# Optimization experiments

Measured on AMD Instinct MI355X. Metric: run time of the kernel, lower is better.

The kernel has to match this reference:

```python
import jax, jax.numpy as jnp
import numpy as np

B, S = 16, 512
IN_DIM, ATTN_DIM, DEPTH, HEADS, DH = 512, 512, 4, 8, 64
CB_DIM, CB_SIZE, MAX_SEQ = 64, 8192, 544


def _ln(x, g, b):
    mu = x.mean(-1, keepdims=True)
    v = ((x - mu) ** 2).mean(-1, keepdims=True)
    return (x - mu) / jnp.sqrt(v + 1e-5) * g + b


def setup_inputs() -> dict:
    key = jax.random.key(0)
    ks = jax.random.split(key, 16)
    sc = 0.02
    d = {
        "x": jax.random.normal(ks[0], (B, S, IN_DIM), jnp.float32),
        "w_in": jax.random.normal(ks[1], (IN_DIM, ATTN_DIM), jnp.float32) * sc,
        "b_in": jnp.zeros((ATTN_DIM,), jnp.float32),
        "pos_emb": jax.random.normal(ks[2], (MAX_SEQ, ATTN_DIM), jnp.float32) * sc,
        "ln1_g": jnp.ones((DEPTH, ATTN_DIM), jnp.float32),
        "ln1_b": jnp.zeros((DEPTH, ATTN_DIM), jnp.float32),
        "wq": jax.random.normal(ks[3], (DEPTH, ATTN_DIM, ATTN_DIM), jnp.float32) * sc,
        "wk": jax.random.normal(ks[4], (DEPTH, ATTN_DIM, ATTN_DIM), jnp.float32) * sc,
        "wv": jax.random.normal(ks[5], (DEPTH, ATTN_DIM, ATTN_DIM), jnp.float32) * sc,
        "wo": jax.random.normal(ks[6], (DEPTH, ATTN_DIM, ATTN_DIM), jnp.float32) * sc,
        "ln2_g": jnp.ones((DEPTH, ATTN_DIM), jnp.float32),
        "ln2_b": jnp.zeros((DEPTH, ATTN_DIM), jnp.float32),
        "ff_w1": jax.random.normal(ks[7], (DEPTH, ATTN_DIM, 4 * ATTN_DIM), jnp.float32) * sc,
        "ff_b1": jnp.zeros((DEPTH, 4 * ATTN_DIM), jnp.float32),
        "ff_w2": jax.random.normal(ks[8], (DEPTH, 4 * ATTN_DIM, ATTN_DIM), jnp.float32) * sc,
        "ff_b2": jnp.zeros((DEPTH, ATTN_DIM), jnp.float32),
        "lnf_g": jnp.ones((ATTN_DIM,), jnp.float32),
        "lnf_b": jnp.zeros((ATTN_DIM,), jnp.float32),
        "w_out": jax.random.normal(ks[9], (ATTN_DIM, CB_DIM), jnp.float32) * sc,
        "b_out": jnp.zeros((CB_DIM,), jnp.float32),
        "codebook": jax.random.normal(ks[10], (CB_SIZE, CB_DIM), jnp.float32),
    }
    return d


def _attn(h, wq, wk, wv, wo):
    b, s, _ = h.shape
    q = jnp.einsum('bsd,de->bse', h, wq).reshape(b, s, HEADS, DH)
    k = jnp.einsum('bsd,de->bse', h, wk).reshape(b, s, HEADS, DH)
    v = jnp.einsum('bsd,de->bse', h, wv).reshape(b, s, HEADS, DH)
    scores = jnp.einsum('bqhd,bkhd->bhqk', q, k) * (DH ** -0.5)
    a = jax.nn.softmax(scores, axis=-1)
    o = jnp.einsum('bhqk,bkhd->bqhd', a, v).reshape(b, s, ATTN_DIM)
    return jnp.einsum('bse,ed->bsd', o, wo)


def reference(x, w_in, b_in, pos_emb, ln1_g, ln1_b, wq, wk, wv, wo,
              ln2_g, ln2_b, ff_w1, ff_b1, ff_w2, ff_b2, lnf_g, lnf_b,
              w_out, b_out, codebook):
    s = x.shape[1]
    # ContinuousTransformerWrapper: project in + absolute pos emb
    h = jnp.einsum('bsd,de->bse', x, w_in) + b_in + pos_emb[:s]
    # pre-norm encoder layers: attn + ff, each residual
    for i in range(DEPTH):
        h = h + _attn(_ln(h, ln1_g[i], ln1_b[i]), wq[i], wk[i], wv[i], wo[i])
        g = _ln(h, ln2_g[i], ln2_b[i])
        g = jax.nn.gelu(jnp.einsum('bsd,df->bsf', g, ff_w1[i]) + ff_b1[i])
        h = h + jnp.einsum('bsf,fd->bsd', g, ff_w2[i]) + ff_b2[i]
    h = _ln(h, lnf_g, lnf_b)
    z = jnp.einsum('bsd,dc->bsc', h, w_out) + b_out  # [B,S,CB_DIM]
    # VectorQuantize: euclidean nearest codebook entry
    d2 = (z ** 2).sum(-1, keepdims=True) - 2.0 * jnp.einsum('bsc,kc->bsk', z, codebook) \
         + (codebook ** 2).sum(-1)  # [B,S,CB_SIZE]
    idx = jnp.argmin(d2, axis=-1)
    q = codebook[idx]  # [B,S,CB_DIM]
    commit_loss = jnp.mean((jax.lax.stop_gradient(q) - z) ** 2)  # commitment_weight=1.0
    q_st = z + jax.lax.stop_gradient(q - z)  # straight-through
    return q_st.sum(axis=1), commit_loss
```

## Files before the change

### kernel.cpp

```cpp
#include <hip/hip_runtime.h>
#include <cmath>

#define BATCH 16
#define SEQ 512
#define DMODEL 512
#define NDEPTH 4
#define NHEADS 8
#define DHEAD 64
#define DFF 2048
#define CBD 64
#define CBS 8192
#define MROWS (BATCH * SEQ)

typedef unsigned short u16;
typedef __attribute__((ext_vector_type(8))) short short8;
typedef __attribute__((ext_vector_type(4))) float f32x4;
typedef __attribute__((ext_vector_type(4))) unsigned short u16x4;

__device__ __forceinline__ u16 f2bf(float f) {
    unsigned u = __float_as_uint(f);
    u += 0x7fff + ((u >> 16) & 1);
    return (u16)(u >> 16);
}
__device__ __forceinline__ float bf2f(u16 h) {
    return __uint_as_float(((unsigned)h) << 16);
}

__device__ __forceinline__ void async16(u16* lds, const u16* g) {
    __builtin_amdgcn_global_load_lds(
        (const __attribute__((address_space(1))) unsigned int*)g,
        (__attribute__((address_space(3))) unsigned int*)lds, 16, 0, 0);
}

__device__ __forceinline__ float gelu_tanh(float u) {
    float t = fmaf(0.07135481627f * u, u * u, 1.5957691216f * u);
    return u / (1.0f + __expf(-t));
}

__global__ void zero_kernel(float* __restrict__ p, int n) {
    int i = blockIdx.x * 256 + threadIdx.x;
    if (i < n) p[i] = 0.0f;
}

__global__ void cbn_kernel(const float* __restrict__ cb, float* __restrict__ cbn) {
    int c = blockIdx.x * 256 + threadIdx.x;
    if (c >= CBS) return;
    const float* row = cb + (size_t)c * CBD;
    float s = 0.0f;
#pragma unroll
    for (int d = 0; d < CBD; ++d) s += row[d] * row[d];
    cbn[c] = s;
}

__global__ __launch_bounds__(256) void wtrans_kernel(
    const float* __restrict__ W, u16* __restrict__ Th, u16* __restrict__ Tl,
    int K, int N, long inLS, long outLS) {
    __shared__ float t[32][33];
    const float* Ws = W + (size_t)blockIdx.z * inLS;
    u16* Tho = Th + (size_t)blockIdx.z * outLS;
    u16* Tlo = Tl + (size_t)blockIdx.z * outLS;
    int n0 = blockIdx.x * 32, k0 = blockIdx.y * 32;
    int tx = threadIdx.x & 31, ty = threadIdx.x >> 5;
#pragma unroll
    for (int r = ty; r < 32; r += 8) t[r][tx] = Ws[(size_t)(k0 + r) * N + n0 + tx];
    __syncthreads();
#pragma unroll
    for (int r = ty; r < 32; r += 8) {
        float v = t[tx][r];
        size_t o = (size_t)(n0 + r) * K + k0 + tx;
        u16 hh = f2bf(v);
        Tho[o] = hh;
        Tlo[o] = f2bf(v - bf2f(hh));
    }
}

__global__ __launch_bounds__(256) void vtrans_kernel(
    const u16* __restrict__ Qh, const u16* __restrict__ Ql,
    u16* __restrict__ VTh, u16* __restrict__ VTl) {
    __shared__ u16 t[64][68];
    int s0 = blockIdx.x * 64;
    int hh = blockIdx.y;
    int b = blockIdx.z & 15, plane = blockIdx.z >> 4;
    const u16* src = (plane ? Ql : Qh) + ((size_t)(16 + hh) * MROWS) * 64;
    u16* dst = (plane ? VTl : VTh);
    int tid = threadIdx.x;
    int rr = tid >> 4, c4 = (tid & 15) * 4;
#pragma unroll
    for (int i = 0; i < 4; ++i) {
        int r = rr + i * 16;
        const u16* p = src + (size_t)(b * SEQ + s0 + r) * 64 + c4;
        *(u16x4*)(&t[r][c4]) = *(const u16x4*)p;
    }
    __syncthreads();
#pragma unroll
    for (int i = 0; i < 4; ++i) {
        int r = rr + i * 16;
        u16x4 v;
        v.x = t[c4 + 0][r]; v.y = t[c4 + 1][r]; v.z = t[c4 + 2][r]; v.w = t[c4 + 3][r];
        *(u16x4*)(dst + (size_t)b * SEQ * DMODEL + (size_t)(hh * 64 + r) * SEQ + s0 + c4) = v;
    }
}

__global__ void split_kernel(const float* __restrict__ X, u16* __restrict__ H,
                             u16* __restrict__ L, int n) {
    int i = blockIdx.x * 256 + threadIdx.x;
    if (i < n) {
        float v = X[i];
        u16 hh = f2bf(v);
        H[i] = hh;
        L[i] = f2bf(v - bf2f(hh));
    }
}

__global__ __launch_bounds__(256) void ln_kernel(
    const float* __restrict__ X,
    const float* __restrict__ C0, const float* __restrict__ C1,
    const float* __restrict__ bias2, const float* __restrict__ pos2,
    float* __restrict__ Xout,
    float* __restrict__ Y, u16* __restrict__ Yh, u16* __restrict__ Yl,
    const float* __restrict__ g, const float* __restrict__ b) {
    int row  = blockIdx.x * 4 + (threadIdx.x >> 6);
    int lane = threadIdx.x & 63;
    float v[8];
    float s = 0.0f;
#pragma unroll
    for (int j = 0; j < 8; ++j) {
        int d = lane + j * 64;
        size_t o = (size_t)row * DMODEL + d;
        float t = X ? X[o] : 0.0f;
        if (C0)    t += C0[o] + C1[o];
        if (bias2) t += bias2[d];
        if (pos2)  t += pos2[(size_t)(row & (SEQ - 1)) * DMODEL + d];
        v[j] = t;
        if (Xout) Xout[o] = t;
        s += t;
    }
#pragma unroll
    for (int off = 32; off; off >>= 1) s += __shfl_xor(s, off);
    float mu  = s * (1.0f / DMODEL);
    float var = 0.0f;
#pragma unroll
    for (int j = 0; j < 8; ++j) { float d = v[j] - mu; var += d * d; }
#pragma unroll
    for (int off = 32; off; off >>= 1) var += __shfl_xor(var, off);
    float r = rsqrtf(var * (1.0f / DMODEL) + 1e-5f);
#pragma unroll
    for (int j = 0; j < 8; ++j) {
        int d = lane + j * 64;
        float y = (v[j] - mu) * r * g[d] + b[d];
        size_t o = (size_t)row * DMODEL + d;
        if (Y) Y[o] = y;
        if (Yh) {
            u16 hh = f2bf(y);
            Yh[o] = hh;
            Yl[o] = f2bf(y - bf2f(hh));
        }
    }
}

__global__ __launch_bounds__(256) void gemm3_kernel(
    const u16* __restrict__ Ah, const u16* __restrict__ Al,
    const u16* __restrict__ Bh, const u16* __restrict__ Bl,
    float* __restrict__ Cf, u16* __restrict__ Ch, u16* __restrict__ Cl,
    const float* __restrict__ bias, const float* __restrict__ res,
    const float* __restrict__ pos, int M, int N, int K, int gelu,
    float* __restrict__ Cs0, float* __restrict__ Cs1, int kslice, int qkvscatter) {
    __shared__ __align__(16) u16 AsH[128 * 64];
    __shared__ __align__(16) u16 AsL[128 * 64];
    __shared__ __align__(16) u16 BsH[128 * 64];
    __shared__ __align__(16) u16 BsL[128 * 64];

    int tid  = threadIdx.x;
    int w    = tid >> 6, lane = tid & 63;
    int wr   = w >> 1, wc = w & 1;
    int quad = lane >> 4, l16 = lane & 15;
    int m0   = blockIdx.x * 128;
    int n0   = blockIdx.y * 128;
    int ksA  = (kslice > 0) ? blockIdx.z * kslice : 0;
    int ksB  = (kslice > 0) ? ksA + kslice : K;

    f32x4 acc[4][4];
#pragma unroll
    for (int i = 0; i < 4; ++i)
#pragma unroll
        for (int j = 0; j < 4; ++j) acc[i][j] = (f32x4){0.f, 0.f, 0.f, 0.f};

    int ldsoff[4];
    size_t goff[4];
#pragma unroll
    for (int r = 0; r < 4; ++r) {
        int cidx = tid + 256 * r;
        int row = cidx >> 3;
        int cg = (cidx & 7) ^ (row & 7);
        ldsoff[r] = cidx * 8;
        goff[r] = (size_t)row * K + cg * 8;
    }

    const u16* AbaseH = Ah + (size_t)m0 * K;
    const u16* AbaseL = Al + (size_t)m0 * K;
    const u16* BbaseH = Bh + (size_t)n0 * K;
    const u16* BbaseL = Bl + (size_t)n0 * K;

    for (int ks = ksA; ks < ksB; ks += 64) {
        __syncthreads();
#pragma unroll
        for (int r = 0; r < 4; ++r) {
            size_t g = goff[r] + ks;
            async16(&AsH[ldsoff[r]], AbaseH + g);
            async16(&AsL[ldsoff[r]], AbaseL + g);
            async16(&BsH[ldsoff[r]], BbaseH + g);
            async16(&BsL[ldsoff[r]], BbaseL + g);
        }
        __syncthreads();
#pragma unroll
        for (int s = 0; s < 2; ++s) {
            short8 afh[4], afl[4];
#pragma unroll
            for (int i = 0; i < 4; ++i) {
                int row = wr * 64 + i * 16 + l16;
                int off = row * 64 + (((s << 2) | quad) ^ (row & 7)) * 8;
                afh[i] = *(const short8*)&AsH[off];
                afl[i] = *(const short8*)&AsL[off];
            }
#pragma unroll
            for (int j = 0; j < 4; ++j) {
                int rowb = wc * 64 + j * 16 + l16;
                int offb = rowb * 64 + (((s << 2) | quad) ^ (rowb & 7)) * 8;
                short8 bh = *(const short8*)&BsH[offb];
                short8 bl = *(const short8*)&BsL[offb];
#pragma unroll
                for (int i = 0; i < 4; ++i) {
                    acc[i][j] = __builtin_amdgcn_mfma_f32_16x16x32_bf16(afh[i], bh, acc[i][j], 0, 0, 0);
                    acc[i][j] = __builtin_amdgcn_mfma_f32_16x16x32_bf16(afl[i], bh, acc[i][j], 0, 0, 0);
                    acc[i][j] = __builtin_amdgcn_mfma_f32_16x16x32_bf16(afh[i], bl, acc[i][j], 0, 0, 0);
                }
            }
        }
    }

    float* Cspl = (kslice > 0) ? (blockIdx.z ? Cs1 : Cs0) : nullptr;
    int mbase = m0 + wr * 64;
    int nbase = n0 + wc * 64;
#pragma unroll
    for (int mi = 0; mi < 4; ++mi)
#pragma unroll
        for (int ni = 0; ni < 4; ++ni) {
            f32x4 a = acc[mi][ni];
#pragma unroll
            for (int r = 0; r < 4; ++r) {
                int m = mbase + mi * 16 + quad * 4 + r;
                int n = nbase + ni * 16 + l16;
                float v = a[r];
                size_t o = qkvscatter
                    ? ((size_t)(n >> 6) * M + m) * 64 + (n & 63)
                    : (size_t)m * N + n;
                if (Cspl) { Cspl[o] = v; continue; }
                if (bias) v += bias[n];
                if (pos)  v += pos[(size_t)(m & (SEQ - 1)) * N + n];
                if (res)  v += res[(size_t)m * N + n];
                if (gelu) v = gelu_tanh(v);
                if (Cf) Cf[o] = v;
                if (Ch) {
                    u16 hh = f2bf(v);
                    Ch[o] = hh;
                    Cl[o] = f2bf(v - bf2f(hh));
                }
            }
        }
}

__global__ __launch_bounds__(256) void gemm_kernel(
    const float* __restrict__ A, const float* __restrict__ Bm,
    float* __restrict__ C, const float* __restrict__ bias,
    int M, int N, int K) {
    __shared__ float As[16][68];
    __shared__ float Bs[16][64];
    int tid = threadIdx.x;
    int tx = tid & 15, ty = tid >> 4;
    int a_m = tid >> 2, a_k = (tid & 3) * 4;
    int b_k = tid >> 4, b_n = (tid & 15) * 4;
    const float* Arow = A + (size_t)(blockIdx.x * 64 + a_m) * K;
    const float* Bcol = Bm + (size_t)blockIdx.y * 64 + b_n;
    float acc[4][4] = {};
    for (int k0 = 0; k0 < K; k0 += 16) {
        float4 av = *(const float4*)(Arow + k0 + a_k);
        float4 bv = *(const float4*)(Bcol + (size_t)(k0 + b_k) * N);
        __syncthreads();
        As[a_k + 0][a_m] = av.x; As[a_k + 1][a_m] = av.y;
        As[a_k + 2][a_m] = av.z; As[a_k + 3][a_m] = av.w;
        *(float4*)(&Bs[b_k][b_n]) = bv;
        __syncthreads();
#pragma unroll
        for (int kk = 0; kk < 16; ++kk) {
            float4 a4 = *(const float4*)(&As[kk][ty * 4]);
            float4 b4 = *(const float4*)(&Bs[kk][tx * 4]);
            float ar[4] = {a4.x, a4.y, a4.z, a4.w};
            float br[4] = {b4.x, b4.y, b4.z, b4.w};
#pragma unroll
            for (int i = 0; i < 4; ++i)
#pragma unroll
                for (int j = 0; j < 4; ++j) acc[i][j] = fmaf(ar[i], br[j], acc[i][j]);
        }
    }
    int m0 = blockIdx.x * 64 + ty * 4;
    int n0 = blockIdx.y * 64 + tx * 4;
#pragma unroll
    for (int i = 0; i < 4; ++i) {
        float vv[4];
#pragma unroll
        for (int j = 0; j < 4; ++j) {
            float t = acc[i][j];
            if (bias) t += bias[n0 + j];
            vv[j] = t;
        }
        *(float4*)(C + (size_t)(m0 + i) * N + n0) = make_float4(vv[0], vv[1], vv[2], vv[3]);
    }
}

__global__ __launch_bounds__(256) void attn_flash_kernel(
    const u16* __restrict__ QKh, const u16* __restrict__ QKl,
    const u16* __restrict__ VTh, const u16* __restrict__ VTl,
    u16* __restrict__ Oh, u16* __restrict__ Ol) {
    int bh = blockIdx.x & 127;
    int qt = blockIdx.x >> 7;
    int bb = bh >> 3, hh = bh & 7;

    __shared__ __align__(16) float Pw[4][16 * 68];

    int tid = threadIdx.x;
    int w = tid >> 6, lane = tid & 63;
    int quad = lane >> 4, l16 = lane & 15;
    int qtile = qt * 4 + w;
    float* P = Pw[w];

    const u16* qrh = QKh + ((size_t)hh * MROWS + bb * SEQ + qtile * 16 + l16) * 64 + quad * 8;
    const u16* qrl = QKl + ((size_t)hh * MROWS + bb * SEQ + qtile * 16 + l16) * 64 + quad * 8;
    short8 Qh0 = *(const short8*)qrh;
    short8 Qh1 = *(const short8*)(qrh + 32);
    short8 Ql0 = *(const short8*)qrl;
    short8 Ql1 = *(const short8*)(qrl + 32);

    float m[4] = {-1e30f, -1e30f, -1e30f, -1e30f};
    float lsum[4] = {0.f, 0.f, 0.f, 0.f};
    f32x4 acc[4];
#pragma unroll
    for (int dt = 0; dt < 4; ++dt) acc[dt] = (f32x4){0.f, 0.f, 0.f, 0.f};

    const u16* KbH = QKh + ((size_t)(8 + hh) * MROWS + bb * SEQ) * 64;
    const u16* KbL = QKl + ((size_t)(8 + hh) * MROWS + bb * SEQ) * 64;
    const u16* VbH = VTh + (size_t)bb * SEQ * DMODEL + (size_t)(hh * 64) * SEQ;
    const u16* VbL = VTl + (size_t)bb * SEQ * DMODEL + (size_t)(hh * 64) * SEQ;

    for (int kt = 0; kt < 8; ++kt) {
        int kb = kt * 64;
        f32x4 st[4];
#pragma unroll
        for (int s = 0; s < 4; ++s) {
            const u16* kh = KbH + (size_t)(kb + s * 16 + l16) * 64 + quad * 8;
            const u16* kl = KbL + (size_t)(kb + s * 16 + l16) * 64 + quad * 8;
            short8 Kh0 = *(const short8*)kh;
            short8 Kh1 = *(const short8*)(kh + 32);
            short8 Kl0 = *(const short8*)kl;
            short8 Kl1 = *(const short8*)(kl + 32);
            f32x4 a = (f32x4){0.f, 0.f, 0.f, 0.f};
            a = __builtin_amdgcn_mfma_f32_16x16x32_bf16(Qh0, Kh0, a, 0, 0, 0);
            a = __builtin_amdgcn_mfma_f32_16x16x32_bf16(Qh1, Kh1, a, 0, 0, 0);
            a = __builtin_amdgcn_mfma_f32_16x16x32_bf16(Ql0, Kh0, a, 0, 0, 0);
            a = __builtin_amdgcn_mfma_f32_16x16x32_bf16(Ql1, Kh1, a, 0, 0, 0);
            a = __builtin_amdgcn_mfma_f32_16x16x32_bf16(Qh0, Kl0, a, 0, 0, 0);
            a = __builtin_amdgcn_mfma_f32_16x16x32_bf16(Qh1, Kl1, a, 0, 0, 0);
            st[s] = a * 0.125f;
        }
        float alpha[4];
#pragma unroll
        for (int r = 0; r < 4; ++r) {
            float mx = fmaxf(fmaxf(st[0][r], st[1][r]), fmaxf(st[2][r], st[3][r]));
#pragma unroll
            for (int off = 8; off; off >>= 1) mx = fmaxf(mx, __shfl_xor(mx, off));
            float mn = fmaxf(m[r], mx);
            alpha[r] = __expf(m[r] - mn);
            m[r] = mn;
        }
#pragma unroll
        for (int r = 0; r < 4; ++r) {
            float rs = 0.f;
#pragma unroll
            for (int s = 0; s < 4; ++s) {
                float p = __expf(st[s][r] - m[r]);
                st[s][r] = p;
                rs += p;
            }
#pragma unroll
            for (int off = 8; off; off >>= 1) rs += __shfl_xor(rs, off);
            lsum[r] = lsum[r] * alpha[r] + rs;
        }
#pragma unroll
        for (int dt = 0; dt < 4; ++dt)
#pragma unroll
            for (int r = 0; r < 4; ++r) acc[dt][r] *= alpha[r];
#pragma unroll
        for (int s = 0; s < 4; ++s)
#pragma unroll
            for (int r = 0; r < 4; ++r)
                P[(quad * 4 + r) * 68 + s * 16 + l16] = st[s][r];
        short8 ph[2], pl[2];
#pragma unroll
        for (int ks = 0; ks < 2; ++ks) {
            const float* src = &P[l16 * 68 + ks * 32 + quad * 8];
            f32x4 a0 = *(const f32x4*)src;
            f32x4 a1 = *(const f32x4*)(src + 4);
            float v[8] = {a0[0], a0[1], a0[2], a0[3], a1[0], a1[1], a1[2], a1[3]};
#pragma unroll
            for (int j = 0; j < 8; ++j) {
                u16 hv = f2bf(v[j]);
                ph[ks][j] = (short)hv;
                pl[ks][j] = (short)f2bf(v[j] - bf2f(hv));
            }
        }
#pragma unroll
        for (int dt = 0; dt < 4; ++dt) {
            const u16* vh = VbH + (size_t)(dt * 16 + l16) * SEQ + kb + quad * 8;
            const u16* vl = VbL + (size_t)(dt * 16 + l16) * SEQ + kb + quad * 8;
            short8 Vh0 = *(const short8*)vh;
            short8 Vh1 = *(const short8*)(vh + 32);
            short8 Vl0 = *(const short8*)vl;
            short8 Vl1 = *(const short8*)(vl + 32);
            acc[dt] = __builtin_amdgcn_mfma_f32_16x16x32_bf16(ph[0], Vh0, acc[dt], 0, 0, 0);
            acc[dt] = __builtin_amdgcn_mfma_f32_16x16x32_bf16(ph[1], Vh1, acc[dt], 0, 0, 0);
            acc[dt] = __builtin_amdgcn_mfma_f32_16x16x32_bf16(pl[0], Vh0, acc[dt], 0, 0, 0);
            acc[dt] = __builtin_amdgcn_mfma_f32_16x16x32_bf16(pl[1], Vh1, acc[dt], 0, 0, 0);
            acc[dt] = __builtin_amdgcn_mfma_f32_16x16x32_bf16(ph[0], Vl0, acc[dt], 0, 0, 0);
            acc[dt] = __builtin_amdgcn_mfma_f32_16x16x32_bf16(ph[1], Vl1, acc[dt], 0, 0, 0);
        }
    }

#pragma unroll
    for (int r = 0; r < 4; ++r) {
        float inv = 1.0f / lsum[r];
        size_t rowoff = (size_t)(bb * SEQ + qtile * 16 + quad * 4 + r) * DMODEL + hh * 64;
#pragma unroll
        for (int dt = 0; dt < 4; ++dt) {
            float v = acc[dt][r] * inv;
            u16 hv = f2bf(v);
            Oh[rowoff + dt * 16 + l16] = hv;
            Ol[rowoff + dt * 16 + l16] = f2bf(v - bf2f(hv));
        }
    }
}

__global__ __launch_bounds__(256) void vq3_kernel(
    const float* __restrict__ Z, const u16* __restrict__ Zh, const u16* __restrict__ Zl,
    const u16* __restrict__ CBh, const u16* __restrict__ CBl,
    const float* __restrict__ CB, const float* __restrict__ CBN,
    float* __restrict__ out) {
    __shared__ float sbest[4][16];
    __shared__ int sidx[4][16];
    __shared__ int ibest[16];
    __shared__ float psum[4][64];
    __shared__ float cl4[4];

    int tid = threadIdx.x;
    int w = tid >> 6, lane = tid & 63;
    int quad = lane >> 4, l16 = lane & 15;
    int row0 = blockIdx.x * 16;

    const u16* zph = Zh + (size_t)(row0 + l16) * CBD + quad * 8;
    const u16* zpl = Zl + (size_t)(row0 + l16) * CBD + quad * 8;
    short8 Z0h = *(const short8*)zph;
    short8 Z1h = *(const short8*)(zph + 32);
    short8 Z0l = *(const short8*)zpl;
    short8 Z1l = *(const short8*)(zpl + 32);

    float best[4] = {3.4e38f, 3.4e38f, 3.4e38f, 3.4e38f};
    int bidx[4] = {0, 0, 0, 0};

    int cbase = w * (CBS / 4);
#pragma unroll 2
    for (int t = 0; t < CBS / 4; t += 16) {
        int code = cbase + t + l16;
        const u16* cph = CBh + (size_t)code * CBD + quad * 8;
        const u16* cpl = CBl + (size_t)code * CBD + quad * 8;
        short8 C0h = *(const short8*)cph;
        short8 C1h = *(const short8*)(cph + 32);
        short8 C0l = *(const short8*)cpl;
        short8 C1l = *(const short8*)(cpl + 32);
        float cn = CBN[code];
        f32x4 a = (f32x4){0.f, 0.f, 0.f, 0.f};
        a = __builtin_amdgcn_mfma_f32_16x16x32_bf16(Z0h, C0h, a, 0, 0, 0);
        a = __builtin_amdgcn_mfma_f32_16x16x32_bf16(Z1h, C1h, a, 0, 0, 0);
        a = __builtin_amdgcn_mfma_f32_16x16x32_bf16(Z0l, C0h, a, 0, 0, 0);
        a = __builtin_amdgcn_mfma_f32_16x16x32_bf16(Z1l, C1h, a, 0, 0, 0);
        a = __builtin_amdgcn_mfma_f32_16x16x32_bf16(Z0h, C0l, a, 0, 0, 0);
        a = __builtin_amdgcn_mfma_f32_16x16x32_bf16(Z1h, C1l, a, 0, 0, 0);
#pragma unroll
        for (int r = 0; r < 4; ++r) {
            float s = cn - 2.0f * a[r];
            if (s < best[r]) { best[r] = s; bidx[r] = code; }
        }
    }
#pragma unroll
    for (int off = 8; off; off >>= 1) {
#pragma unroll
        for (int r = 0; r < 4; ++r) {
            float ov = __shfl_xor(best[r], off);
            int oi = __shfl_xor(bidx[r], off);
            if (ov < best[r] || (ov == best[r] && oi < bidx[r])) { best[r] = ov; bidx[r] = oi; }
        }
    }
    if (l16 == 0) {
#pragma unroll
        for (int r = 0; r < 4; ++r) {
            sbest[w][quad * 4 + r] = best[r];
            sidx[w][quad * 4 + r] = bidx[r];
        }
    }
    __syncthreads();
    if (tid < 16) {
        float bv = sbest[0][tid];
        int bi = sidx[0][tid];
#pragma unroll
        for (int ww = 1; ww < 4; ++ww) {
            float ov = sbest[ww][tid];
            int oi = sidx[ww][tid];
            if (ov < bv || (ov == bv && oi < bi)) { bv = ov; bi = oi; }
        }
        ibest[tid] = bi;
    }
    __syncthreads();

    int d2 = lane;
    float qacc = 0.0f, closs = 0.0f;
#pragma unroll
    for (int j = 0; j < 4; ++j) {
        int r2 = w * 4 + j;
        int bi = ibest[r2];
        float q = CB[(size_t)bi * CBD + d2];
        float z = Z[(size_t)(row0 + r2) * CBD + d2];
        qacc += q;
        float df = q - z;
        closs += df * df;
    }
    psum[w][d2] = qacc;
#pragma unroll
    for (int off = 32; off; off >>= 1) closs += __shfl_xor(closs, off);
    if (d2 == 0) cl4[w] = closs;
    __syncthreads();
    if (tid < 64) {
        float t = psum[0][tid] + psum[1][tid] + psum[2][tid] + psum[3][tid];
        int b = row0 >> 9;
        atomicAdd(out + b * 64 + tid, t);
    }
    if (tid == 0)
        atomicAdd(out + 1024, (cl4[0] + cl4[1] + cl4[2] + cl4[3]) * (1.0f / (float)(MROWS * CBD)));
}

extern "C" void kernel_launch(void* const* d_in, const int* in_sizes, int n_in,
                              void* d_out, int out_size, void* d_ws, size_t ws_size,
                              hipStream_t stream) {
    const float* x    = (const float*)d_in[0];
    const float* w_in = (const float*)d_in[1];
    const float* b_in = (const float*)d_in[2];
    const float* pos  = (const float*)d_in[3];
    const float* ln1g = (const float*)d_in[4];
    const float* ln1b = (const float*)d_in[5];
    const float* wq   = (const float*)d_in[6];
    const float* wk   = (const float*)d_in[7];
    const float* wv   = (const float*)d_in[8];
    const float* wo   = (const float*)d_in[9];
    const float* ln2g = (const float*)d_in[10];
    const float* ln2b = (const float*)d_in[11];
    const float* ffw1 = (const float*)d_in[12];
    const float* ffb1 = (const float*)d_in[13];
    const float* ffw2 = (const float*)d_in[14];
    const float* ffb2 = (const float*)d_in[15];
    const float* lnfg = (const float*)d_in[16];
    const float* lnfb = (const float*)d_in[17];
    const float* wout = (const float*)d_in[18];
    const float* bout = (const float*)d_in[19];
    const float* cb   = (const float*)d_in[20];
    float* out = (float*)d_out;

    const size_t MD  = (size_t)MROWS * DMODEL;
    const size_t MQ  = (size_t)MROWS * 1536;
    const size_t MF  = (size_t)MROWS * DFF;

    float* ws   = (float*)d_ws;
    float* h    = ws;
    float* t0   = h + MD;
    float* big  = t0 + MD;
    float* zb   = big + MF;
    float* cbn  = zb + (size_t)MROWS * CBD;
    u16* cbh    = (u16*)(cbn + CBS);
    u16* cbl    = cbh + (size_t)CBS * CBD;
    u16* t0h    = (u16*)(cbh + 2 * (size_t)CBS * CBD);
    u16* t0l    = t0h + MD;
    u16* wb     = t0l + MD;

    u16* qkvh = (u16*)big;
    u16* qkvl = qkvh + MQ;
    u16* obh  = qkvl + MQ;
    u16* obl  = obh + MD;
    u16* xh   = obh;
    u16* xl   = obl;
    u16* fmh  = (u16*)big;
    u16* fml  = fmh + MF;
    u16* zbh  = (u16*)big;
    u16* zbl  = zbh + (size_t)MROWS * CBD;

    const size_t S_WIN  = (size_t)DMODEL * DMODEL;
    const size_t S_QKV  = (size_t)1536 * DMODEL * NDEPTH;
    const size_t S_WO   = S_WIN * NDEPTH;
    const size_t S_FF1  = (size_t)DFF * DMODEL * NDEPTH;
    const size_t S_FF2  = S_FF1;
    u16* winT_h = wb;
    u16* winT_l = winT_h + S_WIN;
    u16* qkvT_h = winT_l + S_WIN;
    u16* qkvT_l = qkvT_h + S_QKV;
    u16* woT_h  = qkvT_l + S_QKV;
    u16* woT_l  = woT_h + S_WO;
    u16* ff1T_h = woT_l + S_WO;
    u16* ff1T_l = ff1T_h + S_FF1;
    u16* ff2T_h = ff1T_l + S_FF1;
    u16* ff2T_l = ff2T_h + S_FF2;
    u16* VTh = ff2T_l + S_FF2;
    u16* VTl = VTh + (size_t)BATCH * SEQ * DMODEL;
    float* spK0 = (float*)(VTl + (size_t)BATCH * SEQ * DMODEL);
    float* spK1 = spK0 + MD;

    dim3 blk(256);

    zero_kernel<<<dim3((out_size + 255) / 256), blk, 0, stream>>>(out, out_size);
    cbn_kernel<<<dim3(CBS / 256), blk, 0, stream>>>(cb, cbn);
    split_kernel<<<dim3((int)(CBS * CBD / 256)), blk, 0, stream>>>(cb, cbh, cbl, CBS * CBD);

    wtrans_kernel<<<dim3(16, 16, 1), blk, 0, stream>>>(w_in, winT_h, winT_l, DMODEL, DMODEL, 0, 0);
    wtrans_kernel<<<dim3(16, 16, NDEPTH), blk, 0, stream>>>(
        wq, qkvT_h, qkvT_l, DMODEL, DMODEL, (long)DMODEL * DMODEL, (long)1536 * DMODEL);
    wtrans_kernel<<<dim3(16, 16, NDEPTH), blk, 0, stream>>>(
        wk, qkvT_h + (size_t)512 * DMODEL, qkvT_l + (size_t)512 * DMODEL,
        DMODEL, DMODEL, (long)DMODEL * DMODEL, (long)1536 * DMODEL);
    wtrans_kernel<<<dim3(16, 16, NDEPTH), blk, 0, stream>>>(
        wv, qkvT_h + (size_t)1024 * DMODEL, qkvT_l + (size_t)1024 * DMODEL,
        DMODEL, DMODEL, (long)DMODEL * DMODEL, (long)1536 * DMODEL);
    wtrans_kernel<<<dim3(16, 16, NDEPTH), blk, 0, stream>>>(
        wo, woT_h, woT_l, DMODEL, DMODEL, (long)DMODEL * DMODEL, (long)DMODEL * DMODEL);
    wtrans_kernel<<<dim3(DFF / 32, 16, NDEPTH), blk, 0, stream>>>(
        ffw1, ff1T_h, ff1T_l, DMODEL, DFF, (long)DMODEL * DFF, (long)DFF * DMODEL);
    wtrans_kernel<<<dim3(16, DFF / 32, NDEPTH), blk, 0, stream>>>(
        ffw2, ff2T_h, ff2T_l, DFF, DMODEL, (long)DFF * DMODEL, (long)DMODEL * DFF);

    split_kernel<<<dim3((int)(MD / 256)), blk, 0, stream>>>(x, xh, xl, (int)MD);

    gemm3_kernel<<<dim3(MROWS / 128, DMODEL / 128, 2), blk, 0, stream>>>(
        xh, xl, winT_h, winT_l, nullptr, nullptr, nullptr, nullptr, nullptr, nullptr,
        MROWS, DMODEL, DMODEL, 0, spK0, spK1, 256, 0);

    for (int l = 0; l < NDEPTH; ++l) {
        ln_kernel<<<dim3(MROWS / 4), blk, 0, stream>>>(
            (l == 0) ? nullptr : h, spK0, spK1,
            (l == 0) ? b_in : (ffb2 + (size_t)(l - 1) * DMODEL),
            (l == 0) ? pos : nullptr, h,
            nullptr, t0h, t0l, ln1g + l * DMODEL, ln1b + l * DMODEL);
        gemm3_kernel<<<dim3(MROWS / 128, 1536 / 128, 1), blk, 0, stream>>>(
            t0h, t0l, qkvT_h + (size_t)l * 1536 * DMODEL, qkvT_l + (size_t)l * 1536 * DMODEL,
            nullptr, qkvh, qkvl, nullptr, nullptr, nullptr, MROWS, 1536, DMODEL, 0,
            nullptr, nullptr, 0, 1);
        vtrans_kernel<<<dim3(8, 8, 32), blk, 0, stream>>>(qkvh, qkvl, VTh, VTl);
        attn_flash_kernel<<<dim3(1024), blk, 0, stream>>>(
            qkvh, qkvl, VTh, VTl, obh, obl);
        gemm3_kernel<<<dim3(MROWS / 128, DMODEL / 128, 2), blk, 0, stream>>>(
            obh, obl, woT_h + (size_t)l * S_WIN, woT_l + (size_t)l * S_WIN,
            nullptr, nullptr, nullptr, nullptr, nullptr, nullptr,
            MROWS, DMODEL, DMODEL, 0, spK0, spK1, 256, 0);
        ln_kernel<<<dim3(MROWS / 4), blk, 0, stream>>>(
            h, spK0, spK1, nullptr, nullptr, h,
            nullptr, t0h, t0l, ln2g + l * DMODEL, ln2b + l * DMODEL);
        gemm3_kernel<<<dim3(MROWS / 128, DFF / 128, 1), blk, 0, stream>>>(
            t0h, t0l, ff1T_h + (size_t)l * DFF * DMODEL, ff1T_l + (size_t)l * DFF * DMODEL,
            nullptr, fmh, fml, ffb1 + l * DFF, nullptr, nullptr, MROWS, DFF, DMODEL, 1,
            nullptr, nullptr, 0, 0);
        gemm3_kernel<<<dim3(MROWS / 128, DMODEL / 128, 2), blk, 0, stream>>>(
            fmh, fml, ff2T_h + (size_t)l * DFF * DMODEL, ff2T_l + (size_t)l * DFF * DMODEL,
            nullptr, nullptr, nullptr, nullptr, nullptr, nullptr,
            MROWS, DMODEL, DFF, 0, spK0, spK1, 1024, 0);
    }

    ln_kernel<<<dim3(MROWS / 4), blk, 0, stream>>>(
        h, spK0, spK1, ffb2 + (size_t)3 * DMODEL, nullptr, nullptr,
        t0, nullptr, nullptr, lnfg, lnfb);
    gemm_kernel<<<dim3(MROWS / 64, 1), blk, 0, stream>>>(t0, wout, zb, bout, MROWS, CBD, DMODEL);
    split_kernel<<<dim3((int)((size_t)MROWS * CBD / 256)), blk, 0, stream>>>(
        zb, zbh, zbl, MROWS * CBD);
    vq3_kernel<<<dim3(MROWS / 16), blk, 0, stream>>>(zb, zbh, zbl, cbh, cbl, cb, cbn, out);
}
```

Before: 1.791 ms.

## Split attention key range across two wave groups and merge partial softmax

The attention kernel now launches 512 threads per block, so two groups of four waves process the same query tiles over disjoint halves of the key sequence. The second group writes its partial accumulators, running max and sum to shared memory, and the first group merges them with a log-sum-exp rescale before writing output. This is meant to shorten the serial key loop per wave and raise parallelism and latency hiding. The cost is more threads per block, two block barriers and a shared-memory combine step.

Measured after the change: 2.346 ms. +31.0%, slower.

```diff
diff --git a/kernel.cpp b/kernel.cpp
--- a/kernel.cpp
+++ b/kernel.cpp
@@ -317,7 +317,7 @@
     }
 }
 
-__global__ __launch_bounds__(256) void attn_flash_kernel(
+__global__ __launch_bounds__(512, 8) void attn_flash_kernel(
     const u16* __restrict__ QKh, const u16* __restrict__ QKl,
     const u16* __restrict__ VTh, const u16* __restrict__ VTl,
     u16* __restrict__ Oh, u16* __restrict__ Ol) {
@@ -325,12 +325,13 @@
     int qt = blockIdx.x >> 7;
     int bb = bh >> 3, hh = bh & 7;
 
-    __shared__ __align__(16) float Pw[4][16 * 68];
+    __shared__ __align__(16) float Pw[8][16 * 68];
 
     int tid = threadIdx.x;
     int w = tid >> 6, lane = tid & 63;
+    int half = w >> 2, tix = w & 3;
     int quad = lane >> 4, l16 = lane & 15;
-    int qtile = qt * 4 + w;
+    int qtile = qt * 4 + tix;
     float* P = Pw[w];
 
     const u16* qrh = QKh + ((size_t)hh * MROWS + bb * SEQ + qtile * 16 + l16) * 64 + quad * 8;
@@ -351,7 +352,8 @@
     const u16* VbH = VTh + (size_t)bb * SEQ * DMODEL + (size_t)(hh * 64) * SEQ;
     const u16* VbL = VTl + (size_t)bb * SEQ * DMODEL + (size_t)(hh * 64) * SEQ;
 
-    for (int kt = 0; kt < 8; ++kt) {
+    int kt0 = half * 4;
+    for (int kt = kt0; kt < kt0 + 4; ++kt) {
         int kb = kt * 64;
         f32x4 st[4];
 #pragma unroll
@@ -434,16 +436,38 @@
         }
     }
 
-#pragma unroll
-    for (int r = 0; r < 4; ++r) {
-        float inv = 1.0f / lsum[r];
-        size_t rowoff = (size_t)(bb * SEQ + qtile * 16 + quad * 4 + r) * DMODEL + hh * 64;
-#pragma unroll
-        for (int dt = 0; dt < 4; ++dt) {
-            float v = acc[dt][r] * inv;
-            u16 hv = f2bf(v);
-            Oh[rowoff + dt * 16 + l16] = hv;
-            Ol[rowoff + dt * 16 + l16] = f2bf(v - bf2f(hv));
+    __syncthreads();
+    float* comb = &Pw[0][0];
+    if (half == 1) {
+        float* c = comb + ((size_t)tix * 64 + lane) * 25;
+#pragma unroll
+        for (int dt = 0; dt < 4; ++dt)
+#pragma unroll
+            for (int r = 0; r < 4; ++r) c[dt * 4 + r] = acc[dt][r];
+#pragma unroll
+        for (int r = 0; r < 4; ++r) {
+            c[16 + r] = m[r];
+            c[20 + r] = lsum[r];
+        }
+    }
+    __syncthreads();
+    if (half == 0) {
+        const float* c = comb + ((size_t)tix * 64 + lane) * 25;
+#pragma unroll
+        for (int r = 0; r < 4; ++r) {
+            float mB = c[16 + r], lB = c[20 + r];
+            float mn = fmaxf(m[r], mB);
+            float aA = __expf(m[r] - mn);
+            float aB = __expf(mB - mn);
+            float linv = 1.0f / (lsum[r] * aA + lB * aB);
+            size_t rowoff = (size_t)(bb * SEQ + qtile * 16 + quad * 4 + r) * DMODEL + hh * 64;
+#pragma unroll
+            for (int dt = 0; dt < 4; ++dt) {
+                float v = (acc[dt][r] * aA + c[dt * 4 + r] * aB) * linv;
+                u16 hv = f2bf(v);
+                Oh[rowoff + dt * 16 + l16] = hv;
+                Ol[rowoff + dt * 16 + l16] = f2bf(v - bf2f(hv));
+            }
         }
     }
 }
@@ -666,7 +690,7 @@
             nullptr, qkvh, qkvl, nullptr, nullptr, nullptr, MROWS, 1536, DMODEL, 0,
             nullptr, nullptr, 0, 1);
         vtrans_kernel<<<dim3(8, 8, 32), blk, 0, stream>>>(qkvh, qkvl, VTh, VTl);
-        attn_flash_kernel<<<dim3(1024), blk, 0, stream>>>(
+        attn_flash_kernel<<<dim3(1024), dim3(512), 0, stream>>>(
             qkvh, qkvl, VTh, VTl, obh, obl);
         gemm3_kernel<<<dim3(MROWS / 128, DMODEL / 128, 2), blk, 0, stream>>>(
             obh, obl, woT_h + (size_t)l * S_WIN, woT_l + (size_t)l * S_WIN,
```

## Split attention over two key halves and merge partials in separate kernel

Applied to the files above, without the earlier changes.

The flash attention kernel now runs 2048 blocks, each handling half of the key range, and writes unnormalized fp32 partial outputs plus running max and sum to scratch buffers. A new merge kernel combines the two halves with log-sum-exp rescaling and emits the hi/lo bf16 split output. This doubles the grid to raise occupancy and parallelism across CUs, at the cost of extra fp32 scratch traffic and one more kernel launch per layer. A launch bound hint of 8 waves is also added.

Measured after the change: 2.512 ms. 40.3% more time.

```diff
diff --git a/kernel.cpp b/kernel.cpp
--- a/kernel.cpp
+++ b/kernel.cpp
@@ -317,12 +317,13 @@
     }
 }
 
-__global__ __launch_bounds__(256) void attn_flash_kernel(
+__global__ __launch_bounds__(256, 8) void attn_flash_kernel(
     const u16* __restrict__ QKh, const u16* __restrict__ QKl,
     const u16* __restrict__ VTh, const u16* __restrict__ VTl,
-    u16* __restrict__ Oh, u16* __restrict__ Ol) {
+    float* __restrict__ Sp0, float* __restrict__ Sp1, float* __restrict__ ML) {
     int bh = blockIdx.x & 127;
-    int qt = blockIdx.x >> 7;
+    int qt = (blockIdx.x >> 7) & 7;
+    int half = blockIdx.x >> 10;
     int bb = bh >> 3, hh = bh & 7;
 
     __shared__ __align__(16) float Pw[4][16 * 68];
@@ -351,7 +352,8 @@
     const u16* VbH = VTh + (size_t)bb * SEQ * DMODEL + (size_t)(hh * 64) * SEQ;
     const u16* VbL = VTl + (size_t)bb * SEQ * DMODEL + (size_t)(hh * 64) * SEQ;
 
-    for (int kt = 0; kt < 8; ++kt) {
+    int kt0 = half * 4;
+    for (int kt = kt0; kt < kt0 + 4; ++kt) {
         int kb = kt * 64;
         f32x4 st[4];
 #pragma unroll
@@ -434,17 +436,42 @@
         }
     }
 
+    float* Opart = half ? Sp1 : Sp0;
 #pragma unroll
     for (int r = 0; r < 4; ++r) {
-        float inv = 1.0f / lsum[r];
-        size_t rowoff = (size_t)(bb * SEQ + qtile * 16 + quad * 4 + r) * DMODEL + hh * 64;
-#pragma unroll
-        for (int dt = 0; dt < 4; ++dt) {
-            float v = acc[dt][r] * inv;
-            u16 hv = f2bf(v);
-            Oh[rowoff + dt * 16 + l16] = hv;
-            Ol[rowoff + dt * 16 + l16] = f2bf(v - bf2f(hv));
-        }
+        int grow = bb * SEQ + qtile * 16 + quad * 4 + r;
+        size_t rowoff = (size_t)grow * DMODEL + hh * 64;
+#pragma unroll
+        for (int dt = 0; dt < 4; ++dt)
+            Opart[rowoff + dt * 16 + l16] = acc[dt][r];
+        if (l16 == 0) {
+            size_t mo = ((size_t)(half * MROWS + grow) * NHEADS + hh) * 2;
+            ML[mo + 0] = m[r];
+            ML[mo + 1] = lsum[r];
+        }
+    }
+}
+
+__global__ __launch_bounds__(256) void attn_merge_kernel(
+    const float* __restrict__ Sp0, const float* __restrict__ Sp1,
+    const float* __restrict__ ML,
+    u16* __restrict__ Oh, u16* __restrict__ Ol) {
+    int row = blockIdx.x * 4 + (threadIdx.x >> 6);
+    int lane = threadIdx.x & 63;
+#pragma unroll
+    for (int j = 0; j < 8; ++j) {
+        size_t o = (size_t)row * DMODEL + j * 64 + lane;
+        size_t mo0 = ((size_t)row * NHEADS + j) * 2;
+        size_t mo1 = ((size_t)(MROWS + row) * NHEADS + j) * 2;
+        float m0 = ML[mo0 + 0], l0 = ML[mo0 + 1];
+        float m1 = ML[mo1 + 0], l1 = ML[mo1 + 1];
+        float M = fmaxf(m0, m1);
+        float a0 = __expf(m0 - M), a1 = __expf(m1 - M);
+        float inv = 1.0f / (l0 * a0 + l1 * a1);
+        float v = (Sp0[o] * a0 + Sp1[o] * a1) * inv;
+        u16 hv = f2bf(v);
+        Oh[o] = hv;
+        Ol[o] = f2bf(v - bf2f(hv));
     }
 }
 
@@ -626,6 +653,7 @@
     u16* VTl = VTh + (size_t)BATCH * SEQ * DMODEL;
     float* spK0 = (float*)(VTl + (size_t)BATCH * SEQ * DMODEL);
     float* spK1 = spK0 + MD;
+    float* mlbuf = t0;
 
     dim3 blk(256);
 
@@ -666,8 +694,10 @@
             nullptr, qkvh, qkvl, nullptr, nullptr, nullptr, MROWS, 1536, DMODEL, 0,
             nullptr, nullptr, 0, 1);
         vtrans_kernel<<<dim3(8, 8, 32), blk, 0, stream>>>(qkvh, qkvl, VTh, VTl);
-        attn_flash_kernel<<<dim3(1024), blk, 0, stream>>>(
-            qkvh, qkvl, VTh, VTl, obh, obl);
+        attn_flash_kernel<<<dim3(2048), blk, 0, stream>>>(
+            qkvh, qkvl, VTh, VTl, spK0, spK1, mlbuf);
+        attn_merge_kernel<<<dim3(MROWS / 4), blk, 0, stream>>>(
+            spK0, spK1, mlbuf, obh, obl);
         gemm3_kernel<<<dim3(MROWS / 128, DMODEL / 128, 2), blk, 0, stream>>>(
             obh, obl, woT_h + (size_t)l * S_WIN, woT_l + (size_t)l * S_WIN,
             nullptr, nullptr, nullptr, nullptr, nullptr, nullptr,
```
